# Optimization experiments

Measured on AMD Instinct MI355X. Metric: run time of the kernel, lower is better.

The kernel has to match this reference:

```python
import jax, jax.numpy as jnp
import numpy as np

N_LAST = 100000
M_CUR = 50000
E = 1600000
F_IN = 64
H = 64  # hidden width of both MLPs


def setup_inputs() -> dict:
    key = jax.random.key(0)
    ks = jax.random.split(key, 12)
    last_coors = jax.random.normal(ks[0], (N_LAST, 3), dtype=jnp.float32)
    last_features = jax.random.normal(ks[1], (N_LAST, F_IN), dtype=jnp.float32)
    current_coors = jax.random.normal(ks[2], (M_CUR, 3), dtype=jnp.float32)
    cur_idx = jax.random.randint(ks[3], (E,), 0, M_CUR, dtype=jnp.int32)
    last_idx = jax.random.randint(ks[4], (E,), 0, N_LAST, dtype=jnp.int32)
    edge = jnp.stack([cur_idx, last_idx], axis=0)
    d_in = F_IN + 3  # 67: features concat relative coords
    def lin(k, fan_in, fan_out):
        bound = 1.0 / np.sqrt(fan_in)
        kw, kb = jax.random.split(k)
        W = jax.random.uniform(kw, (fan_in, fan_out), jnp.float32, -bound, bound)
        b = jax.random.uniform(kb, (fan_out,), jnp.float32, -bound, bound)
        return W, b
    W1, b1 = lin(ks[5], d_in, H)
    W2, b2 = lin(ks[6], H, H)
    W3, b3 = lin(ks[7], H, H)
    W4, b4 = lin(ks[8], H, H)
    return {"last_coors": last_coors, "last_features": last_features,
            "current_coors": current_coors, "edge": edge,
            "W1": W1, "b1": b1, "W2": W2, "b2": b2,
            "W3": W3, "b3": b3, "W4": W4, "b4": b4}


def reference(last_coors, last_features, current_coors, edge,
              W1, b1, W2, b2, W3, b3, W4, b4):
    cur_idx = edge[0]   # [E] indices into current level
    last_idx = edge[1]  # [E] indices into last level
    m = current_coors.shape[0]
    # gather + relative coords concat -> [E, F_IN+3]
    rel = last_coors[last_idx] - current_coors[cur_idx]
    x = jnp.concatenate([last_features[last_idx], rel], axis=1)
    # in_linear: two Linear+ReLU layers
    x = jax.nn.relu(x @ W1 + b1)
    x = jax.nn.relu(x @ W2 + b2)
    # scatter_max into zero-initialized output (torch uses out=zeros, so
    # empty segments stay 0 and max is taken against 0 baseline)
    agg = jax.ops.segment_max(x, cur_idx, num_segments=m)
    agg = jnp.maximum(agg, 0.0)
    # out_linear: two Linear+ReLU layers
    y = jax.nn.relu(agg @ W3 + b3)
    y = jax.nn.relu(y @ W4 + b4)
    return y
```

## Files before the change

kernel.cpp:

```cpp
#include <hip/hip_runtime.h>
#include <hip/hip_fp16.h>

#define FIN 64
#define HH 64
#define BLK 128
#define CIW 32
#define CIWB 5
#define T1 16384
#define RST 65

typedef _Float16 h2v __attribute__((ext_vector_type(2)));
typedef _Float16 f16x8 __attribute__((ext_vector_type(8)));
typedef float f32x4 __attribute__((ext_vector_type(4)));
union U4F { uint4 u; f16x8 h; };

__device__ __forceinline__ unsigned pack2(float x, float y) {
    __half2 h = __floats2half2_rn(x, y);
    union { __half2 h; unsigned u; } z; z.h = h;
    return z.u;
}
__device__ __forceinline__ float2 unpack2(unsigned u) {
    union { unsigned u; __half2 h; } z; z.u = u;
    return __half22float2(z.h);
}
__device__ __forceinline__ float fdot2f(unsigned a, unsigned b, float c) {
#if __has_builtin(__builtin_amdgcn_fdot2)
    union { unsigned u; h2v h; } za, zb; za.u = a; zb.u = b;
    return __builtin_amdgcn_fdot2(za.h, zb.h, c, false);
#else
    float2 fa = unpack2(a), fb = unpack2(b);
    return fmaf(fa.x, fb.x, fmaf(fa.y, fb.y, c));
#endif
}

__device__ __forceinline__ void dot2_layer(const unsigned* lds, int t,
        const unsigned* __restrict__ wp, const float* __restrict__ bias, float* h) {
    #pragma unroll
    for (int j = 0; j < 64; ++j) h[j] = bias[j];
    #pragma unroll 1
    for (int c = 0; c < 8; ++c) {
        uint4 hp = *reinterpret_cast<const uint4*>(&lds[(size_t)t * 32 + ((c ^ (t & 7)) << 2)]);
        const unsigned* w0 = wp + (4 * c + 0) * 64;
        const unsigned* w1 = wp + (4 * c + 1) * 64;
        const unsigned* w2 = wp + (4 * c + 2) * 64;
        const unsigned* w3 = wp + (4 * c + 3) * 64;
        #pragma unroll
        for (int j = 0; j < 64; ++j) {
            float a = fdot2f(hp.x, w0[j], h[j]);
            a = fdot2f(hp.y, w1[j], a);
            a = fdot2f(hp.z, w2[j], a);
            h[j] = fdot2f(hp.w, w3[j], a);
        }
    }
}

__global__ void zero_init(float* agg, int nagg, int* counts, int ncnt) {
    int i = blockIdx.x * blockDim.x + threadIdx.x;
    int stride = gridDim.x * blockDim.x;
    for (int k = i; k < nagg; k += stride) agg[k] = 0.f;
    for (int k = i; k < ncnt; k += stride) counts[k] = 0;
}

__global__ __launch_bounds__(256) void histpack(
    const int* __restrict__ edge, int* bcnt, int E, int NBUK, int NB1,
    const float* __restrict__ W1, const float* __restrict__ W2,
    const float* __restrict__ W3, const float* __restrict__ W4, unsigned* wp) {
    extern __shared__ int lh[];
    int b = blockIdx.x, t = threadIdx.x;
    if (b < NB1) {
        for (int j = t; j < NBUK; j += 256) lh[j] = 0;
        __syncthreads();
        int lo = b * T1, hi = min(lo + T1, E);
        for (int e = lo + t; e < hi; e += 256) atomicAdd(&lh[edge[e] >> CIWB], 1);
        __syncthreads();
        for (int j = t; j < NBUK; j += 256) {
            int c = lh[j];
            if (c) atomicAdd(&bcnt[j], c);
        }
    } else {
        int i = (b - NB1) * 256 + t;
        if (i >= 4 * 2048) return;
        int m = i >> 11, r = i & 2047;
        if (m == 1) {
            int tile = r >> 8;
            int l    = (r >> 2) & 63;
            int p    = r & 3;
            int ni = tile & 3, ks = tile >> 2;
            int col = ni * 16 + (l & 15);
            int k0  = ks * 32 + ((l >> 4) << 3) + 2 * p;
            wp[i] = pack2(W2[k0 * 64 + col], W2[(k0 + 1) * 64 + col]);
        } else {
            int kk = r >> 6, j = r & 63;
            const float* W = (m == 0) ? W1 : (m == 2) ? W3 : W4;
            wp[i] = pack2(W[(2 * kk) * 64 + j], W[(2 * kk + 1) * 64 + j]);
        }
    }
}

__global__ __launch_bounds__(1024) void scan_buckets(const int* __restrict__ bcnt,
                                                     int* bbase, int* bres,
                                                     int NBUK, int E) {
    const int T = 1024;
    int t = threadIdx.x;
    int C = (NBUK + T - 1) / T;
    int lo = t * C, hi = min(lo + C, NBUK);
    int s = 0;
    for (int i = lo; i < hi; ++i) s += bcnt[i];
    __shared__ int ss[T];
    ss[t] = s;
    __syncthreads();
    for (int off = 1; off < T; off <<= 1) {
        int v = (t >= off) ? ss[t - off] : 0;
        __syncthreads();
        ss[t] += v;
        __syncthreads();
    }
    int run = (t == 0) ? 0 : ss[t - 1];
    for (int i = lo; i < hi; ++i) {
        bbase[i] = run;
        bres[i] = run;
        run += bcnt[i];
    }
    if (t == 0) bbase[NBUK] = E;
}

__global__ __launch_bounds__(256) void scatter_prepass(
    const int* __restrict__ edge, int* bres, unsigned* bin, int E, int NBUK, int NB1,
    const float* __restrict__ last_features, const unsigned* __restrict__ w1p,
    const float* __restrict__ b1, uint4* pre1, int N) {
    extern __shared__ unsigned shd[];
    int b = blockIdx.x, t = threadIdx.x;
    if (b < NB1) {
        int* lh = (int*)shd;
        int* lofs = lh + NBUK;
        for (int j = t; j < NBUK; j += 256) lh[j] = 0;
        __syncthreads();
        int lo = b * T1, hi = min(lo + T1, E);
        for (int e = lo + t; e < hi; e += 256) atomicAdd(&lh[edge[e] >> CIWB], 1);
        __syncthreads();
        for (int j = t; j < NBUK; j += 256) {
            int c = lh[j];
            lofs[j] = c ? atomicAdd(&bres[j], c) : 0;
            lh[j] = 0;
        }
        __syncthreads();
        for (int e = lo + t; e < hi; e += 256) {
            int ci = edge[e];
            int bk = ci >> CIWB;
            int p = lofs[bk] + atomicAdd(&lh[bk], 1);
            bin[p] = (unsigned)(ci & (CIW - 1)) | ((unsigned)edge[E + e] << CIWB);
        }
    } else {
        int r = (b - NB1) * 256 + t;
        if (r >= N) return;

        const float4* xr = reinterpret_cast<const float4*>(last_features + (size_t)r * FIN);
        float4 f[16];
        #pragma unroll
        for (int i = 0; i < 16; ++i) f[i] = xr[i];

        #pragma unroll
        for (int c = 0; c < 8; ++c) {
            uint4 o;
            o.x = pack2(f[2 * c].x, f[2 * c].y);
            o.y = pack2(f[2 * c].z, f[2 * c].w);
            o.z = pack2(f[2 * c + 1].x, f[2 * c + 1].y);
            o.w = pack2(f[2 * c + 1].z, f[2 * c + 1].w);
            *reinterpret_cast<uint4*>(&shd[(size_t)t * 32 + ((c ^ (t & 7)) << 2)]) = o;
        }

        float h[64];
        dot2_layer(shd, t, w1p, b1, h);

        uint4* out = pre1 + (size_t)r * 8;
        #pragma unroll
        for (int c = 0; c < 8; ++c) {
            uint4 o;
            o.x = pack2(h[8 * c + 0], h[8 * c + 1]);
            o.y = pack2(h[8 * c + 2], h[8 * c + 3]);
            o.z = pack2(h[8 * c + 4], h[8 * c + 5]);
            o.w = pack2(h[8 * c + 6], h[8 * c + 7]);
            out[c] = o;
        }
    }
}

__global__ __launch_bounds__(64, 2) void edge_mfma_fused(
    const float* __restrict__ last_coors,
    const float* __restrict__ current_coors,
    const unsigned* __restrict__ bin,
    const uint4* __restrict__ pre1,
    const float* __restrict__ W1,
    const float* __restrict__ b2,
    const unsigned* __restrict__ w2f,
    const int* __restrict__ bbase,
    float* agg, int M, int NBUK)
{
    __shared__ unsigned Ast[64 * 32];
    __shared__ int rmxi[CIW * RST];

    int bkt = blockIdx.x, t = threadIdx.x;
    int lo = bkt * CIW;
    int start = bbase[bkt], end = bbase[bkt + 1];

    for (int i = t; i < CIW * RST; i += 64) rmxi[i] = 0;

    f16x8 bf[2][4];
    #pragma unroll
    for (int ks = 0; ks < 2; ++ks)
        #pragma unroll
        for (int ni = 0; ni < 4; ++ni) {
            U4F u;
            u.u = *reinterpret_cast<const uint4*>(w2f + (size_t)((ks * 4 + ni) * 64 + t) * 4);
            bf[ks][ni] = u.h;
        }
    float bb[4];
    #pragma unroll
    for (int ni = 0; ni < 4; ++ni) bb[ni] = b2[ni * 16 + (t & 15)];

    const float* rw = W1 + 64 * 64;

    #pragma unroll 1
    for (int s = start; s < end; s += 64) {
        int nE = min(64, end - s);

        uint4 q[8] = {};
        float r0 = 0.f, r1 = 0.f, r2 = 0.f;
        int ci = lo;
        if (t < nE) {
            unsigned bv = bin[s + t];
            ci = lo + (int)(bv & (CIW - 1));
            int li = (int)(bv >> CIWB);
            const uint4* pr = pre1 + (size_t)li * 8;
            #pragma unroll
            for (int i = 0; i < 8; ++i) q[i] = pr[i];
            r0 = last_coors[3 * li + 0] - current_coors[3 * ci + 0];
            r1 = last_coors[3 * li + 1] - current_coors[3 * ci + 1];
            r2 = last_coors[3 * li + 2] - current_coors[3 * ci + 2];
        }

        #pragma unroll
        for (int c = 0; c < 8; ++c) {
            unsigned qc[4] = {q[c].x, q[c].y, q[c].z, q[c].w};
            unsigned oc[4];
            #pragma unroll
            for (int p = 0; p < 4; ++p) {
                int j0 = 8 * c + 2 * p;
                float2 v = unpack2(qc[p]);
                v.x = fmaf(r0, rw[j0],     fmaf(r1, rw[64 + j0],     fmaf(r2, rw[128 + j0],     v.x)));
                v.y = fmaf(r0, rw[j0 + 1], fmaf(r1, rw[64 + j0 + 1], fmaf(r2, rw[128 + j0 + 1], v.y)));
                oc[p] = pack2(fmaxf(v.x, 0.f), fmaxf(v.y, 0.f));
            }
            uint4 o; o.x = oc[0]; o.y = oc[1]; o.z = oc[2]; o.w = oc[3];
            *reinterpret_cast<uint4*>(&Ast[(size_t)t * 32 + ((c ^ (t & 7)) << 2)]) = o;
        }

        f32x4 acc[4][4];
        #pragma unroll
        for (int ni = 0; ni < 4; ++ni)
            #pragma unroll
            for (int mi = 0; mi < 4; ++mi)
                acc[mi][ni] = (f32x4){bb[ni], bb[ni], bb[ni], bb[ni]};

        #pragma unroll
        for (int ks = 0; ks < 2; ++ks) {
            #pragma unroll
            for (int mi = 0; mi < 4; ++mi) {
                int row = mi * 16 + (t & 15);
                int ch  = (ks * 4 + (t >> 4)) ^ (row & 7);
                U4F a;
                a.u = *reinterpret_cast<const uint4*>(&Ast[(size_t)row * 32 + (ch << 2)]);
                #pragma unroll
                for (int ni = 0; ni < 4; ++ni)
                    acc[mi][ni] = __builtin_amdgcn_mfma_f32_16x16x32_f16(
                        a.h, bf[ks][ni], acc[mi][ni], 0, 0, 0);
            }
        }

        #pragma unroll
        for (int mi = 0; mi < 4; ++mi) {
            #pragma unroll
            for (int r = 0; r < 4; ++r) {
                int row = mi * 16 + ((t >> 4) << 2) + r;
                int cir = __shfl(ci, row);
                if (row < nE) {
                    int* dst = &rmxi[(cir - lo) * RST + (t & 15)];
                    #pragma unroll
                    for (int ni = 0; ni < 4; ++ni)
                        atomicMax(&dst[ni * 16], __float_as_int(acc[mi][ni][r]));
                }
            }
        }
    }

    #pragma unroll
    for (int r = 0; r < CIW; ++r) {
        int gr = lo + r;
        if (gr < M) agg[(size_t)gr * 64 + t] = __int_as_float(rmxi[r * RST + t]);
    }
}

__global__ __launch_bounds__(64, 4) void out_mlp2(
    float* data,
    const unsigned* __restrict__ w3p, const float* __restrict__ b3,
    const unsigned* __restrict__ w4p, const float* __restrict__ b4, int M)
{
    __shared__ unsigned lds[64 * 32];
    int t = threadIdx.x;
    int r = blockIdx.x * 64 + t;
    if (r >= M) return;

    const float4* xr = reinterpret_cast<const float4*>(data + (size_t)r * HH);
    float4 f[16];
    #pragma unroll
    for (int i = 0; i < 16; ++i) f[i] = xr[i];

    #pragma unroll
    for (int c = 0; c < 8; ++c) {
        uint4 o;
        o.x = pack2(f[2 * c].x, f[2 * c].y);
        o.y = pack2(f[2 * c].z, f[2 * c].w);
        o.z = pack2(f[2 * c + 1].x, f[2 * c + 1].y);
        o.w = pack2(f[2 * c + 1].z, f[2 * c + 1].w);
        *reinterpret_cast<uint4*>(&lds[(size_t)t * 32 + ((c ^ (t & 7)) << 2)]) = o;
    }

    float h[64];
    dot2_layer(lds, t, w3p, b3, h);

    #pragma unroll
    for (int c = 0; c < 8; ++c) {
        uint4 o;
        o.x = pack2(fmaxf(h[8 * c + 0], 0.f), fmaxf(h[8 * c + 1], 0.f));
        o.y = pack2(fmaxf(h[8 * c + 2], 0.f), fmaxf(h[8 * c + 3], 0.f));
        o.z = pack2(fmaxf(h[8 * c + 4], 0.f), fmaxf(h[8 * c + 5], 0.f));
        o.w = pack2(fmaxf(h[8 * c + 6], 0.f), fmaxf(h[8 * c + 7], 0.f));
        *reinterpret_cast<uint4*>(&lds[(size_t)t * 32 + ((c ^ (t & 7)) << 2)]) = o;
    }

    float h2[64];
    dot2_layer(lds, t, w4p, b4, h2);

    float4* yr = reinterpret_cast<float4*>(data + (size_t)r * HH);
    #pragma unroll
    for (int c = 0; c < 16; ++c) {
        float4 o;
        o.x = fmaxf(h2[4 * c + 0], 0.f);
        o.y = fmaxf(h2[4 * c + 1], 0.f);
        o.z = fmaxf(h2[4 * c + 2], 0.f);
        o.w = fmaxf(h2[4 * c + 3], 0.f);
        yr[c] = o;
    }
}

__global__ void hist_kernel(const int* __restrict__ edge, int* counts, int E) {
    int e = blockIdx.x * blockDim.x + threadIdx.x;
    if (e < E) atomicAdd(&counts[edge[e]], 1);
}

__global__ __launch_bounds__(1024) void scan_kernel(const int* __restrict__ counts,
                                                    int* cursor, int M) {
    const int T = 1024;
    int t = threadIdx.x;
    int C = (M + T - 1) / T;
    int lo = t * C, hi = min(lo + C, M);
    int s = 0;
    for (int i = lo; i < hi; ++i) s += counts[i];
    __shared__ int ss[T];
    ss[t] = s;
    __syncthreads();
    for (int off = 1; off < T; off <<= 1) {
        int v = (t >= off) ? ss[t - off] : 0;
        __syncthreads();
        ss[t] += v;
        __syncthreads();
    }
    int run = (t == 0) ? 0 : ss[t - 1];
    for (int i = lo; i < hi; ++i) {
        cursor[i] = run;
        run += counts[i];
    }
}

__global__ void scatter_kernel(const int* __restrict__ edge, int* cursor,
                               int* sorted, int E) {
    int e = blockIdx.x * blockDim.x + threadIdx.x;
    if (e < E) {
        int p = atomicAdd(&cursor[edge[e]], 1);
        sorted[p] = e;
    }
}

__global__ __launch_bounds__(BLK) void edge_mlp_sorted(
    const float* __restrict__ last_coors, const float* __restrict__ last_features,
    const float* __restrict__ current_coors, const int* __restrict__ edge,
    const int* __restrict__ sorted,
    const float* __restrict__ W1, const float* __restrict__ b1,
    const float* __restrict__ W2, const float* __restrict__ b2,
    float* agg, int E)
{
    __shared__ float hs[BLK][HH];
    __shared__ int cis[BLK];
    __shared__ int runStart[BLK + 1];
    __shared__ int wl[BLK / 64];
    int base = blockIdx.x * BLK, t = threadIdx.x;
    int nE = min(BLK, E - base);
    int ci = -1, li = 0;
    if (t < nE) { int es = sorted[base + t]; ci = edge[es]; li = edge[E + es]; }
    cis[t] = ci;
    if (t < nE) {
        float h1[HH];
        #pragma unroll
        for (int j = 0; j < HH; ++j) h1[j] = b1[j];
        const float4* xr = reinterpret_cast<const float4*>(last_features + (size_t)li * FIN);
        #pragma unroll 1
        for (int c = 0; c < FIN / 4; ++c) {
            float4 v = xr[c];
            const float* w = W1 + (size_t)(4 * c) * HH;
            #pragma unroll
            for (int j = 0; j < HH; ++j)
                h1[j] = fmaf(v.x, w[j], fmaf(v.y, w[HH + j],
                        fmaf(v.z, w[2 * HH + j], fmaf(v.w, w[3 * HH + j], h1[j]))));
        }
        {
            float r0 = last_coors[3 * li + 0] - current_coors[3 * ci + 0];
            float r1 = last_coors[3 * li + 1] - current_coors[3 * ci + 1];
            float r2 = last_coors[3 * li + 2] - current_coors[3 * ci + 2];
            const float* w = W1 + (size_t)64 * HH;
            #pragma unroll
            for (int j = 0; j < HH; ++j)
                h1[j] = fmaf(r0, w[j], fmaf(r1, w[HH + j], fmaf(r2, w[2 * HH + j], h1[j])));
        }
        #pragma unroll
        for (int c = 0; c < HH / 4; ++c) {
            float4 v;
            v.x = fmaxf(h1[4 * c + 0], 0.f); v.y = fmaxf(h1[4 * c + 1], 0.f);
            v.z = fmaxf(h1[4 * c + 2], 0.f); v.w = fmaxf(h1[4 * c + 3], 0.f);
            int cc = (c + t) & 15;
            *reinterpret_cast<float4*>(&hs[t][cc * 4]) = v;
        }
        float h2[HH];
        #pragma unroll
        for (int j = 0; j < HH; ++j) h2[j] = b2[j];
        #pragma unroll 1
        for (int c = 0; c < HH / 4; ++c) {
            int cc = (c + t) & 15;
            float4 v = *reinterpret_cast<const float4*>(&hs[t][cc * 4]);
            const float* w = W2 + (size_t)(4 * c) * HH;
            #pragma unroll
            for (int j = 0; j < HH; ++j)
                h2[j] = fmaf(v.x, w[j], fmaf(v.y, w[HH + j],
                        fmaf(v.z, w[2 * HH + j], fmaf(v.w, w[3 * HH + j], h2[j]))));
        }
        #pragma unroll
        for (int c = 0; c < HH / 4; ++c) {
            float4 v;
            v.x = fmaxf(h2[4 * c + 0], 0.f); v.y = fmaxf(h2[4 * c + 1], 0.f);
            v.z = fmaxf(h2[4 * c + 2], 0.f); v.w = fmaxf(h2[4 * c + 3], 0.f);
            int cc = (c + t) & 15;
            *reinterpret_cast<float4*>(&hs[t][cc * 4]) = v;
        }
    }
    __syncthreads();
    bool leader = (t < nE) && (t == 0 || cis[t] != cis[t - 1]);
    unsigned long long bal = __ballot(leader);
    int lane = t & 63, wid = t >> 6;
    if (lane == 63) wl[wid] = __popcll(bal);
    __syncthreads();
    int nruns = wl[0] + wl[1];
    if (leader) {
        int ord = __popcll(bal & ((1ull << lane) - 1)) + (wid ? wl[0] : 0);
        runStart[ord] = t;
    }
    if (t == 0) runStart[nruns] = nE;
    __syncthreads();
    int col = t & 63, half = t >> 6;
    int* aggi = reinterpret_cast<int*>(agg);
    for (int r = half; r < nruns; r += BLK / 64) {
        int s = runStart[r], e2 = runStart[r + 1];
        int c2 = cis[s];
        float m = 0.f;
        for (int k = s; k < e2; ++k) {
            int cc = ((col >> 2) + k) & 15;
            m = fmaxf(m, hs[k][cc * 4 + (col & 3)]);
        }
        int addr = c2 * HH + col;
        if (s == 0 || e2 == nE) {
            if (m > 0.f) atomicMax(&aggi[addr], __float_as_int(m));
        } else {
            agg[addr] = m;
        }
    }
}

__global__ __launch_bounds__(BLK) void out_mlp_f32(
    float* data, const float* __restrict__ W3, const float* __restrict__ b3,
    const float* __restrict__ W4, const float* __restrict__ b4, int M)
{
    __shared__ float hsm[BLK][HH];
    int r = blockIdx.x * BLK + threadIdx.x;
    if (r >= M) return;
    int t = threadIdx.x;
    const float4* xr = reinterpret_cast<const float4*>(data + (size_t)r * HH);
    float h[HH];
    #pragma unroll
    for (int j = 0; j < HH; ++j) h[j] = b3[j];
    #pragma unroll 1
    for (int c = 0; c < HH / 4; ++c) {
        float4 v = xr[c];
        const float* w = W3 + (size_t)(4 * c) * HH;
        #pragma unroll
        for (int j = 0; j < HH; ++j)
            h[j] = fmaf(v.x, w[j], fmaf(v.y, w[HH + j],
                   fmaf(v.z, w[2 * HH + j], fmaf(v.w, w[3 * HH + j], h[j]))));
    }
    #pragma unroll
    for (int c = 0; c < HH / 4; ++c) {
        float4 v;
        v.x = fmaxf(h[4 * c + 0], 0.f); v.y = fmaxf(h[4 * c + 1], 0.f);
        v.z = fmaxf(h[4 * c + 2], 0.f); v.w = fmaxf(h[4 * c + 3], 0.f);
        int cc = (c + t) & 15;
        *reinterpret_cast<float4*>(&hsm[t][cc * 4]) = v;
    }
    float h2[HH];
    #pragma unroll
    for (int j = 0; j < HH; ++j) h2[j] = b4[j];
    #pragma unroll 1
    for (int c = 0; c < HH / 4; ++c) {
        int cc = (c + t) & 15;
        float4 v = *reinterpret_cast<const float4*>(&hsm[t][cc * 4]);
        const float* w = W4 + (size_t)(4 * c) * HH;
        #pragma unroll
        for (int j = 0; j < HH; ++j)
            h2[j] = fmaf(v.x, w[j], fmaf(v.y, w[HH + j],
                    fmaf(v.z, w[2 * HH + j], fmaf(v.w, w[3 * HH + j], h2[j]))));
    }
    float* yr = data + (size_t)r * HH;
    #pragma unroll
    for (int c = 0; c < HH / 4; ++c) {
        float4 v;
        v.x = fmaxf(h2[4 * c + 0], 0.f); v.y = fmaxf(h2[4 * c + 1], 0.f);
        v.z = fmaxf(h2[4 * c + 2], 0.f); v.w = fmaxf(h2[4 * c + 3], 0.f);
        *reinterpret_cast<float4*>(&yr[4 * c]) = v;
    }
}

extern "C" void kernel_launch(void* const* d_in, const int* in_sizes, int n_in,
                              void* d_out, int out_size, void* d_ws, size_t ws_size,
                              hipStream_t stream) {
    const float* last_coors    = (const float*)d_in[0];
    const float* last_features = (const float*)d_in[1];
    const float* current_coors = (const float*)d_in[2];
    const int*   edge          = (const int*)d_in[3];
    const float* W1 = (const float*)d_in[4];  const float* b1 = (const float*)d_in[5];
    const float* W2 = (const float*)d_in[6];  const float* b2 = (const float*)d_in[7];
    const float* W3 = (const float*)d_in[8];  const float* b3 = (const float*)d_in[9];
    const float* W4 = (const float*)d_in[10]; const float* b4 = (const float*)d_in[11];

    int E = in_sizes[3] / 2;
    int M = in_sizes[2] / 3;
    int N = in_sizes[0] / 3;

    float* agg = (float*)d_out;
    int NBUK = (M + CIW - 1) / CIW;
    int NB1  = (E + T1 - 1) / T1;
    int PPB  = (N + 255) / 256;

    unsigned* ws = (unsigned*)d_ws;
    size_t offBbase = (size_t)NBUK;
    size_t offBres  = offBbase + NBUK + 1;
    size_t offWp    = (offBres + NBUK + 3) & ~(size_t)3;
    size_t offBin   = offWp + 4 * 2048;
    size_t offPre   = (offBin + (size_t)E + 3) & ~(size_t)3;
    size_t need     = (offPre + (size_t)N * 32) * 4;

    if (ws_size >= need && NBUK <= 4096) {
        int* bcnt     = (int*)ws;
        int* bbase    = (int*)(ws + offBbase);
        int* bres     = (int*)(ws + offBres);
        unsigned* wp  = ws + offWp;
        unsigned* bin = ws + offBin;
        uint4* pre1   = (uint4*)(ws + offPre);

        size_t smem2 = 2 * (size_t)NBUK * 4;
        if (smem2 < 32768) smem2 = 32768;

        hipMemsetAsync(bcnt, 0, (size_t)NBUK * 4, stream);
        histpack<<<NB1 + 32, 256, NBUK * 4, stream>>>(edge, bcnt, E, NBUK, NB1,
                                                      W1, W2, W3, W4, wp);
        scan_buckets<<<1, 1024, 0, stream>>>(bcnt, bbase, bres, NBUK, E);
        scatter_prepass<<<NB1 + PPB, 256, smem2, stream>>>(
            edge, bres, bin, E, NBUK, NB1, last_features, wp, b1, pre1, N);
        edge_mfma_fused<<<NBUK, 64, 0, stream>>>(
            last_coors, current_coors, bin, pre1,
            W1, b2, wp + 2048, bbase, agg, M, NBUK);
        out_mlp2<<<(M + 63) / 64, 64, 0, stream>>>(agg, wp + 4096, b3, wp + 6144, b4, M);
    } else {
        int* counts = (int*)ws;
        int* cursor = counts + (M + 1);
        int* sorted = cursor + (M + 1);
        zero_init<<<2048, 256, 0, stream>>>(agg, M * HH, counts, M + 1);
        hist_kernel<<<(E + 255) / 256, 256, 0, stream>>>(edge, counts, E);
        scan_kernel<<<1, 1024, 0, stream>>>(counts, cursor, M);
        scatter_kernel<<<(E + 255) / 256, 256, 0, stream>>>(edge, cursor, sorted, E);
        edge_mlp_sorted<<<(E + BLK - 1) / BLK, BLK, 0, stream>>>(
            last_coors, last_features, current_coors, edge, sorted,
            W1, b1, W2, b2, agg, E);
        out_mlp_f32<<<(M + BLK - 1) / BLK, BLK, 0, stream>>>(agg, W3, b3, W4, b4, M);
    }
}
```

Measured before the change: 209.8 us.

## Use two waves per bucket in edge kernel and restructure prepass layer-1

The edge kernel now runs two wavefronts per bucket, each with its own LDS staging tile, sharing the per-bucket max table through LDS atomics with block syncs. The scatter/prepass kernel moves to 512 threads and computes layer 1 directly from registers with dot2 over packed halves instead of staging features in LDS. The minimum shared-memory size is dropped. The aim is more parallelism per bucket and less LDS traffic, at the cost of higher register pressure and more contention on the shared max table.

```diff
diff --git a/kernel.cpp b/kernel.cpp
--- a/kernel.cpp
+++ b/kernel.cpp
@@ -124,53 +124,60 @@
     if (t == 0) bbase[NBUK] = E;
 }
 
-__global__ __launch_bounds__(256) void scatter_prepass(
+__global__ __launch_bounds__(512) void scatter_prepass(
     const int* __restrict__ edge, int* bres, unsigned* bin, int E, int NBUK, int NB1,
     const float* __restrict__ last_features, const unsigned* __restrict__ w1p,
     const float* __restrict__ b1, uint4* pre1, int N) {
-    extern __shared__ unsigned shd[];
+    extern __shared__ int sh[];
     int b = blockIdx.x, t = threadIdx.x;
     if (b < NB1) {
-        int* lh = (int*)shd;
-        int* lofs = lh + NBUK;
-        for (int j = t; j < NBUK; j += 256) lh[j] = 0;
+        int* lh = sh;
+        int* lofs = sh + NBUK;
+        for (int j = t; j < NBUK; j += 512) lh[j] = 0;
         __syncthreads();
         int lo = b * T1, hi = min(lo + T1, E);
-        for (int e = lo + t; e < hi; e += 256) atomicAdd(&lh[edge[e] >> CIWB], 1);
-        __syncthreads();
-        for (int j = t; j < NBUK; j += 256) {
+        for (int e = lo + t; e < hi; e += 512) atomicAdd(&lh[edge[e] >> CIWB], 1);
+        __syncthreads();
+        for (int j = t; j < NBUK; j += 512) {
             int c = lh[j];
             lofs[j] = c ? atomicAdd(&bres[j], c) : 0;
             lh[j] = 0;
         }
         __syncthreads();
-        for (int e = lo + t; e < hi; e += 256) {
+        for (int e = lo + t; e < hi; e += 512) {
             int ci = edge[e];
             int bk = ci >> CIWB;
             int p = lofs[bk] + atomicAdd(&lh[bk], 1);
             bin[p] = (unsigned)(ci & (CIW - 1)) | ((unsigned)edge[E + e] << CIWB);
         }
     } else {
-        int r = (b - NB1) * 256 + t;
+        int r = (b - NB1) * 512 + t;
         if (r >= N) return;
 
         const float4* xr = reinterpret_cast<const float4*>(last_features + (size_t)r * FIN);
-        float4 f[16];
-        #pragma unroll
-        for (int i = 0; i < 16; ++i) f[i] = xr[i];
-
-        #pragma unroll
+        float h[64];
+        #pragma unroll
+        for (int j = 0; j < 64; ++j) h[j] = b1[j];
+
+        #pragma unroll 1
         for (int c = 0; c < 8; ++c) {
-            uint4 o;
-            o.x = pack2(f[2 * c].x, f[2 * c].y);
-            o.y = pack2(f[2 * c].z, f[2 * c].w);
-            o.z = pack2(f[2 * c + 1].x, f[2 * c + 1].y);
-            o.w = pack2(f[2 * c + 1].z, f[2 * c + 1].w);
-            *reinterpret_cast<uint4*>(&shd[(size_t)t * 32 + ((c ^ (t & 7)) << 2)]) = o;
-        }
-
-        float h[64];
-        dot2_layer(shd, t, w1p, b1, h);
+            float4 fa = xr[2 * c], fb = xr[2 * c + 1];
+            unsigned hp0 = pack2(fa.x, fa.y);
+            unsigned hp1 = pack2(fa.z, fa.w);
+            unsigned hp2 = pack2(fb.x, fb.y);
+            unsigned hp3 = pack2(fb.z, fb.w);
+            const unsigned* w0 = w1p + (4 * c + 0) * 64;
+            const unsigned* w1 = w1p + (4 * c + 1) * 64;
+            const unsigned* w2 = w1p + (4 * c + 2) * 64;
+            const unsigned* w3 = w1p + (4 * c + 3) * 64;
+            #pragma unroll
+            for (int j = 0; j < 64; ++j) {
+                float a = fdot2f(hp0, w0[j], h[j]);
+                a = fdot2f(hp1, w1[j], a);
+                a = fdot2f(hp2, w2[j], a);
+                h[j] = fdot2f(hp3, w3[j], a);
+            }
+        }
 
         uint4* out = pre1 + (size_t)r * 8;
         #pragma unroll
@@ -185,7 +192,7 @@
     }
 }
 
-__global__ __launch_bounds__(64, 2) void edge_mfma_fused(
+__global__ __launch_bounds__(128, 2) void edge_mfma_fused(
     const float* __restrict__ last_coors,
     const float* __restrict__ current_coors,
     const unsigned* __restrict__ bin,
@@ -196,14 +203,18 @@
     const int* __restrict__ bbase,
     float* agg, int M, int NBUK)
 {
-    __shared__ unsigned Ast[64 * 32];
+    __shared__ unsigned AstS[2][64 * 32];
     __shared__ int rmxi[CIW * RST];
 
     int bkt = blockIdx.x, t = threadIdx.x;
+    int w = t >> 6, lane = t & 63;
     int lo = bkt * CIW;
     int start = bbase[bkt], end = bbase[bkt + 1];
 
-    for (int i = t; i < CIW * RST; i += 64) rmxi[i] = 0;
+    for (int i = t; i < CIW * RST; i += 128) rmxi[i] = 0;
+    __syncthreads();
+
+    unsigned* Ast = AstS[w];
 
     f16x8 bf[2][4];
     #pragma unroll
@@ -211,24 +222,24 @@
         #pragma unroll
         for (int ni = 0; ni < 4; ++ni) {
             U4F u;
-            u.u = *reinterpret_cast<const uint4*>(w2f + (size_t)((ks * 4 + ni) * 64 + t) * 4);
+            u.u = *reinterpret_cast<const uint4*>(w2f + (size_t)((ks * 4 + ni) * 64 + lane) * 4);
             bf[ks][ni] = u.h;
         }
     float bb[4];
     #pragma unroll
-    for (int ni = 0; ni < 4; ++ni) bb[ni] = b2[ni * 16 + (t & 15)];
+    for (int ni = 0; ni < 4; ++ni) bb[ni] = b2[ni * 16 + (lane & 15)];
 
     const float* rw = W1 + 64 * 64;
 
     #pragma unroll 1
-    for (int s = start; s < end; s += 64) {
+    for (int s = start + w * 64; s < end; s += 128) {
         int nE = min(64, end - s);
 
         uint4 q[8] = {};
         float r0 = 0.f, r1 = 0.f, r2 = 0.f;
         int ci = lo;
-        if (t < nE) {
-            unsigned bv = bin[s + t];
+        if (lane < nE) {
+            unsigned bv = bin[s + lane];
             ci = lo + (int)(bv & (CIW - 1));
             int li = (int)(bv >> CIWB);
             const uint4* pr = pre1 + (size_t)li * 8;
@@ -252,7 +263,7 @@
                 oc[p] = pack2(fmaxf(v.x, 0.f), fmaxf(v.y, 0.f));
             }
             uint4 o; o.x = oc[0]; o.y = oc[1]; o.z = oc[2]; o.w = oc[3];
-            *reinterpret_cast<uint4*>(&Ast[(size_t)t * 32 + ((c ^ (t & 7)) << 2)]) = o;
+            *reinterpret_cast<uint4*>(&Ast[(size_t)lane * 32 + ((c ^ (lane & 7)) << 2)]) = o;
         }
 
         f32x4 acc[4][4];
@@ -266,8 +277,8 @@
         for (int ks = 0; ks < 2; ++ks) {
             #pragma unroll
             for (int mi = 0; mi < 4; ++mi) {
-                int row = mi * 16 + (t & 15);
-                int ch  = (ks * 4 + (t >> 4)) ^ (row & 7);
+                int row = mi * 16 + (lane & 15);
+                int ch  = (ks * 4 + (lane >> 4)) ^ (row & 7);
                 U4F a;
                 a.u = *reinterpret_cast<const uint4*>(&Ast[(size_t)row * 32 + (ch << 2)]);
                 #pragma unroll
@@ -281,10 +292,10 @@
         for (int mi = 0; mi < 4; ++mi) {
             #pragma unroll
             for (int r = 0; r < 4; ++r) {
-                int row = mi * 16 + ((t >> 4) << 2) + r;
+                int row = mi * 16 + ((lane >> 4) << 2) + r;
                 int cir = __shfl(ci, row);
                 if (row < nE) {
-                    int* dst = &rmxi[(cir - lo) * RST + (t & 15)];
+                    int* dst = &rmxi[(cir - lo) * RST + (lane & 15)];
                     #pragma unroll
                     for (int ni = 0; ni < 4; ++ni)
                         atomicMax(&dst[ni * 16], __float_as_int(acc[mi][ni][r]));
@@ -292,11 +303,11 @@
             }
         }
     }
-
-    #pragma unroll
-    for (int r = 0; r < CIW; ++r) {
-        int gr = lo + r;
-        if (gr < M) agg[(size_t)gr * 64 + t] = __int_as_float(rmxi[r * RST + t]);
+    __syncthreads();
+
+    for (int i = t; i < CIW * 64; i += 128) {
+        int gr = lo + (i >> 6);
+        if (gr < M) agg[(size_t)gr * 64 + (i & 63)] = __int_as_float(rmxi[(i >> 6) * RST + (i & 63)]);
     }
 }
 
@@ -564,7 +575,7 @@
     float* agg = (float*)d_out;
     int NBUK = (M + CIW - 1) / CIW;
     int NB1  = (E + T1 - 1) / T1;
-    int PPB  = (N + 255) / 256;
+    int PPB  = (N + 511) / 512;
 
     unsigned* ws = (unsigned*)d_ws;
     size_t offBbase = (size_t)NBUK;
@@ -583,15 +594,14 @@
         uint4* pre1   = (uint4*)(ws + offPre);
 
         size_t smem2 = 2 * (size_t)NBUK * 4;
-        if (smem2 < 32768) smem2 = 32768;
 
         hipMemsetAsync(bcnt, 0, (size_t)NBUK * 4, stream);
         histpack<<<NB1 + 32, 256, NBUK * 4, stream>>>(edge, bcnt, E, NBUK, NB1,
                                                       W1, W2, W3, W4, wp);
         scan_buckets<<<1, 1024, 0, stream>>>(bcnt, bbase, bres, NBUK, E);
-        scatter_prepass<<<NB1 + PPB, 256, smem2, stream>>>(
+        scatter_prepass<<<NB1 + PPB, 512, smem2, stream>>>(
             edge, bres, bin, E, NBUK, NB1, last_features, wp, b1, pre1, N);
-        edge_mfma_fused<<<NBUK, 64, 0, stream>>>(
+        edge_mfma_fused<<<NBUK, 128, 0, stream>>>(
             last_coors, current_coors, bin, pre1,
             W1, b2, wp + 2048, bbase, agg, M, NBUK);
         out_mlp2<<<(M + 63) / 64, 64, 0, stream>>>(agg, wp + 4096, b3, wp + 6144, b4, M);
```

Result: faster. 199.4 us (-4.9%).
